# Performance work log

Measured on AMD Instinct MI355X. Metric: run time of the kernel, lower is better.

Reference implementation:

```python
import jax, jax.numpy as jnp
import numpy as np

H = 1536      # hidden_size
V = 128       # input_size == output_size (char vocab)
ML = 128      # MAX_LENGTH
SOS = 0


def setup_inputs() -> dict:
    key = jax.random.key(0)
    ks = jax.random.split(key, 16)
    s = 1.0 / np.sqrt(H)
    f = lambda k, shp: jax.random.uniform(k, shp, jnp.float32, -s, s)
    return {
        "input_tensor": jax.random.randint(ks[0], (64,), 0, V),
        "max_length": ML,
        # encoder params
        "emb_enc": f(ks[1], (V, H)),
        "enc_Wih": f(ks[2], (3 * H, H)),
        "enc_Whh": f(ks[3], (3 * H, H)),
        "enc_bih": f(ks[4], (3 * H,)),
        "enc_bhh": f(ks[5], (3 * H,)),
        # decoder params
        "emb_dec": f(ks[6], (V, H)),
        "attn_W": f(ks[7], (ML + 1, 2 * H)),
        "attn_b": f(ks[8], (ML + 1,)),
        "comb_W": f(ks[9], (H, 2 * H)),
        "comb_b": f(ks[10], (H,)),
        "dec_Wih": f(ks[11], (3 * H, H)),
        "dec_Whh": f(ks[12], (3 * H, H)),
        "dec_bih": f(ks[13], (3 * H,)),
        "dec_bhh": f(ks[14], (3 * H,)),
        "out_W": f(ks[15], (V, H)),
        "out_b": jnp.zeros((V,), jnp.float32),
    }


def gru_step(x, h, Wih, Whh, bih, bhh):
    # PyTorch GRUCell math
    gi = Wih @ x + bih
    gh = Whh @ h + bhh
    i_r, i_z, i_n = jnp.split(gi, 3)
    h_r, h_z, h_n = jnp.split(gh, 3)
    r = jax.nn.sigmoid(i_r + h_r)
    z = jax.nn.sigmoid(i_z + h_z)
    n = jnp.tanh(i_n + r * h_n)
    return (1.0 - z) * n + z * h


def reference(input_tensor, max_length, emb_enc, enc_Wih, enc_Whh, enc_bih,
              enc_bhh, emb_dec, attn_W, attn_b, comb_W, comb_b, dec_Wih,
              dec_Whh, dec_bih, dec_bhh, out_W, out_b):
    L = input_tensor.shape[0]

    # ---- encoder: sequential GRU over input tokens ----
    def enc_step(h, tok):
        h = gru_step(emb_enc[tok], h, enc_Wih, enc_Whh, enc_bih, enc_bhh)
        return h, h
    h0 = jnp.zeros((H,), emb_enc.dtype)
    enc_h, enc_outs = jax.lax.scan(enc_step, h0, input_tensor)  # (L, H)
    encoder_outputs = jnp.zeros((max_length + 1, H), emb_enc.dtype).at[:L].set(enc_outs)

    # ---- attention decoder: greedy decode for max_length steps ----
    def dec_step(carry, _):
        h, tok = carry
        emb = emb_dec[tok]                                   # (H,)
        attn_logits = attn_W @ jnp.concatenate([emb, h]) + attn_b
        attn_w = jax.nn.softmax(attn_logits)                 # (ML+1,)
        context = attn_w @ encoder_outputs                   # (H,)
        x = jax.nn.relu(comb_W @ jnp.concatenate([emb, context]) + comb_b)
        h = gru_step(x, h, dec_Wih, dec_Whh, dec_bih, dec_bhh)
        logp = jax.nn.log_softmax(out_W @ h + out_b)         # (V,)
        nxt = jnp.argmax(logp).astype(tok.dtype)
        return (h, nxt), (logp, nxt)

    tok0 = jnp.asarray(SOS, input_tensor.dtype)
    _, (logps, tokens) = jax.lax.scan(dec_step, (enc_h, tok0), None,
                                      length=max_length)
    return logps, tokens  # (ML, V) log-probs, (ML,) greedy token ids
```

## Files before the change

kernel.cpp:

```cpp
#include <hip/hip_runtime.h>
#include <math.h>

#define H     1536
#define H3    4608
#define V     128
#define ML    128
#define MLP1  129
#define LEN   64
#define NBLK  256
#define NTHR  384
#define WPB   6
#define NWAVE (NBLK*WPB)
#define ACC_N    260
#define ACC_ROWS 8
#define ACC_STEP (ACC_ROWS*ACC_N)
#define TA_STRIDE 132

#define SCALEF     1099511627776.0f
#define INV_SCALED 9.094947017729282379150390625e-13

#define OFF_BAR 0
#define OFF_ZB  4096
#define OFF_ACC 10240
#define OFF_HS  2156800
#define OFF_XS  2943232
#define OFF_XE  3729664
#define OFF_GI  4122880
#define OFF_EO  5302528
#define OFF_M   5695744
#define OFF_TA  6088960
#define OFF_TC  6156544
#define OFF_CT  6942976
#define WS_END  8540416
#define MEMSET_BYTES 2156800

__device__ __forceinline__ float uc_ldf(const float* p){
  return __hip_atomic_load(p, __ATOMIC_RELAXED, __HIP_MEMORY_SCOPE_AGENT);
}
__device__ __forceinline__ void uc_stf(float* p, float v){
  __hip_atomic_store(p, v, __ATOMIC_RELAXED, __HIP_MEMORY_SCOPE_AGENT);
}
__device__ __forceinline__ unsigned uc_ldu(const unsigned* p){
  return __hip_atomic_load(p, __ATOMIC_RELAXED, __HIP_MEMORY_SCOPE_AGENT);
}
__device__ __forceinline__ void uc_stu64(unsigned long long* p, unsigned long long v){
  __hip_atomic_store(p, v, __ATOMIC_RELAXED, __HIP_MEMORY_SCOPE_AGENT);
}

__device__ __forceinline__ float wred(float v){
  #pragma unroll
  for(int s=32;s>0;s>>=1) v += __shfl_xor(v, s, 64);
  return v;
}

__device__ __forceinline__ void load6(const float* p, int lane, float4 r[6]){
  const float4* q = (const float4*)p;
  #pragma unroll
  for(int c=0;c<6;c++) r[c] = q[c*64+lane];
}
__device__ __forceinline__ float dot4(const float4 a, const float4 b){
  return a.x*b.x + a.y*b.y + a.z*b.z + a.w*b.w;
}
__device__ __forceinline__ float dot6(const float4 a[6], const float4 b[6]){
  float s=0.f;
  #pragma unroll
  for(int c=0;c<6;c++) s += dot4(a[c], b[c]);
  return s;
}

__device__ __forceinline__ void gbar(unsigned* bar, int rnd){
  __syncthreads();
  if(threadIdx.x==0){
    unsigned* grp  = bar + 32*(1 + (blockIdx.x >> 4));
    unsigned* root = bar;
    unsigned a = __hip_atomic_fetch_add(grp, 1u, __ATOMIC_RELAXED, __HIP_MEMORY_SCOPE_AGENT);
    if((a & 0xFFFFu) == (unsigned)(16*rnd + 15)){
      unsigned ra = __hip_atomic_fetch_add(root, 1u, __ATOMIC_RELAXED, __HIP_MEMORY_SCOPE_AGENT);
      if(ra != (unsigned)(16*rnd + 15)){
        while(uc_ldu(root) < (unsigned)(16*(rnd+1)))
          __builtin_amdgcn_s_sleep(1);
      }
      __hip_atomic_fetch_add(grp, 0x10000u, __ATOMIC_RELAXED, __HIP_MEMORY_SCOPE_AGENT);
    } else {
      while((uc_ldu(grp) >> 16) < (unsigned)(rnd+1))
        __builtin_amdgcn_s_sleep(1);
    }
  }
  __syncthreads();
}

__global__ __launch_bounds__(NTHR, 2)
void seq2seq_kernel(const int* __restrict__ toks,
                    const float* __restrict__ emb_enc,
                    const float* __restrict__ enc_Wih,
                    const float* __restrict__ enc_Whh,
                    const float* __restrict__ enc_bih,
                    const float* __restrict__ enc_bhh,
                    const float* __restrict__ emb_dec,
                    const float* __restrict__ attn_W,
                    const float* __restrict__ attn_b,
                    const float* __restrict__ comb_W,
                    const float* __restrict__ comb_b,
                    const float* __restrict__ dec_Wih,
                    const float* __restrict__ dec_Whh,
                    const float* __restrict__ dec_bih,
                    const float* __restrict__ dec_bhh,
                    const float* __restrict__ out_W,
                    const float* __restrict__ out_b,
                    float* __restrict__ out,
                    char* __restrict__ ws)
{
  const int tid = threadIdx.x, b = blockIdx.x;
  const int lane = tid & 63, w = tid >> 6;
  const int gw = b*WPB + w;
  int rnd = 0;

  unsigned* bar = (unsigned*)ws;
  float* zb = (float*)(ws + OFF_ZB);
  unsigned long long* accseq = (unsigned long long*)(ws + OFF_ACC);
  float* hseq = (float*)(ws + OFF_HS);
  float* xseq = (float*)(ws + OFF_XS);
  float* Xe = (float*)(ws + OFF_XE);
  float* Gi = (float*)(ws + OFF_GI);
  float* EO = (float*)(ws + OFF_EO);
  float* Mm = (float*)(ws + OFF_M);
  float* tA = (float*)(ws + OFF_TA);
  float* tC = (float*)(ws + OFF_TC);
  float* cT = (float*)(ws + OFF_CT);

  __shared__ float smem[WPB*3*H];
  __shared__ float sh[H];
  __shared__ float sx[H];
  __shared__ float scT[WPB*ACC_N];
  __shared__ float sv[ACC_N];
  __shared__ float shc[8];

  for(int idx = b*NTHR + tid; idx < LEN*H; idx += NBLK*NTHR){
    int t = idx / H, k = idx - t*H;
    uc_stf(&Xe[idx], emb_enc[toks[t]*H + k]);
  }
  for(int idx = b*NTHR + tid; idx < H*257; idx += NBLK*NTHR){
    int i = idx / 257, c = idx - i*257;
    float v = (c < MLP1) ? attn_W[(size_t)c*2*H + H + i]
                         : out_W[(size_t)(c-MLP1)*H + i];
    uc_stf(&cT[(size_t)i*ACC_N + c], v);
  }
  gbar(bar, rnd++);

  {
    int r = b*18 + w*3;
    for(int g=0; g<4; g++){
      __syncthreads();
      for(int idx = tid; idx < 16*384; idx += NTHR)
        ((float4*)smem)[idx] = ((const float4*)Xe)[g*16*384 + idx];
      __syncthreads();
      float4 rv0[6], rv1[6], rv2[6];
      load6(enc_Wih + (size_t)r*H,     lane, rv0);
      load6(enc_Wih + (size_t)(r+1)*H, lane, rv1);
      load6(enc_Wih + (size_t)(r+2)*H, lane, rv2);
      float a0[16], a1[16], a2[16];
      #pragma unroll
      for(int t2=0;t2<16;t2++){ a0[t2]=0.f; a1[t2]=0.f; a2[t2]=0.f; }
      #pragma unroll
      for(int c=0;c<6;c++){
        #pragma unroll
        for(int t2=0;t2<16;t2++){
          float4 x = ((float4*)smem)[t2*384 + c*64 + lane];
          a0[t2] += dot4(rv0[c], x);
          a1[t2] += dot4(rv1[c], x);
          a2[t2] += dot4(rv2[c], x);
        }
      }
      float bi0 = enc_bih[r], bi1 = enc_bih[r+1], bi2 = enc_bih[r+2];
      #pragma unroll
      for(int t2=0;t2<16;t2++){
        float s0 = wred(a0[t2]), s1 = wred(a1[t2]), s2 = wred(a2[t2]);
        if(lane==0){
          uc_stf(&Gi[(size_t)(g*16+t2)*H3 + r    ], s0 + bi0);
          uc_stf(&Gi[(size_t)(g*16+t2)*H3 + r + 1], s1 + bi1);
          uc_stf(&Gi[(size_t)(g*16+t2)*H3 + r + 2], s2 + bi2);
        }
      }
    }
  }
  gbar(bar, rnd++);

  {
    int i = gw;
    float4 rv[6]; load6(comb_W + (size_t)i*2*H, lane, rv);
    for(int g=0; g<8; g++){
      __syncthreads();
      for(int idx = tid; idx < 16*384; idx += NTHR)
        ((float4*)smem)[idx] = ((const float4*)emb_dec)[g*16*384 + idx];
      __syncthreads();
      float a0[16];
      #pragma unroll
      for(int t2=0;t2<16;t2++) a0[t2]=0.f;
      #pragma unroll
      for(int c=0;c<6;c++){
        #pragma unroll
        for(int t2=0;t2<16;t2++){
          float4 x = ((float4*)smem)[t2*384 + c*64 + lane];
          a0[t2] += dot4(rv[c], x);
        }
      }
      #pragma unroll
      for(int t2=0;t2<16;t2++){
        float s = wred(a0[t2]);
        if(lane==0) uc_stf(&tC[(size_t)(g*16+t2)*H + i], s);
      }
    }
  }

  for(int task = gw; task < MLP1*V; task += NWAVE){
    int j = task >> 7, v = task & 127;
    float4 av[6]; load6(attn_W + (size_t)j*2*H, lane, av);
    float4 ev[6]; load6(emb_dec + (size_t)v*H, lane, ev);
    float s = wred(dot6(av, ev));
    if(lane==0) uc_stf(&tA[v*TA_STRIDE + j], s);
  }
  gbar(bar, rnd++);

  for(int idx = tid; idx < 18*384; idx += NTHR){
    int row = idx/384, k4 = idx - row*384;
    int w2 = row/3, gate = row - w2*3;
    ((float4*)smem)[idx] =
      ((const float4*)enc_Whh)[((size_t)gate*H + b*WPB + w2)*384 + k4];
  }
  const int i0 = gw;
  float gi0 = Gi[(size_t)lane*H3 + i0];
  float gi1 = Gi[(size_t)lane*H3 + i0 + H];
  float gi2 = Gi[(size_t)lane*H3 + i0 + 2*H];
  float eb0 = enc_bhh[i0], eb1 = enc_bhh[i0+H], eb2 = enc_bhh[i0+2*H];
  __syncthreads();

  for(int t=0; t<LEN; t++){
    const float* hprev = (t==0) ? zb : (EO + (size_t)(t-1)*H);
    ((float4*)sh)[tid] = ((const float4*)hprev)[tid];
    __syncthreads();
    float4 hv[6]; load6(sh, lane, hv);
    float s[3];
    #pragma unroll
    for(int g=0; g<3; g++){
      const float4* sr = (const float4*)smem + (w*3+g)*384;
      float t0=0.f;
      #pragma unroll
      for(int c=0;c<6;c++) t0 += dot4(sr[c*64+lane], hv[c]);
      s[g] = wred(t0);
    }
    float ir = __shfl(gi0, t, 64), iz = __shfl(gi1, t, 64), in_ = __shfl(gi2, t, 64);
    if(lane==0){
      float r = 1.f/(1.f+expf(-(ir + s[0] + eb0)));
      float z = 1.f/(1.f+expf(-(iz + s[1] + eb1)));
      float n = tanhf(in_ + r*(s[2] + eb2));
      float hn = (1.f-z)*n + z*sh[i0];
      uc_stf(&EO[(size_t)t*H + i0], hn);
    }
    gbar(bar, rnd++);
  }

  {
    int i = gw;
    float4 rv[6]; load6(comb_W + (size_t)i*2*H + H, lane, rv);
    for(int g=0; g<4; g++){
      __syncthreads();
      for(int idx = tid; idx < 16*384; idx += NTHR)
        ((float4*)smem)[idx] = ((const float4*)EO)[g*16*384 + idx];
      __syncthreads();
      float a0[16];
      #pragma unroll
      for(int t2=0;t2<16;t2++) a0[t2]=0.f;
      #pragma unroll
      for(int c=0;c<6;c++){
        #pragma unroll
        for(int t2=0;t2<16;t2++){
          float4 x = ((float4*)smem)[t2*384 + c*64 + lane];
          a0[t2] += dot4(rv[c], x);
        }
      }
      #pragma unroll
      for(int t2=0;t2<16;t2++){
        float s = wred(a0[t2]);
        if(lane==0) uc_stf(&Mm[(size_t)i*64 + g*16 + t2], s);
      }
    }
  }

  if(gw < MLP1){
    int j = gw;
    float4 av[6]; load6(attn_W + (size_t)j*2*H + H, lane, av);
    float4 hv[6]; load6(EO + (size_t)(LEN-1)*H, lane, hv);
    float s = wred(dot6(av, hv));
    if(lane==0)
      uc_stu64(&accseq[j], (unsigned long long)(long long)rintf(s*SCALEF));
  }
  for(int idx = tid; idx < 18*384; idx += NTHR){
    int row = idx/384, k4 = idx - row*384;
    int w2 = row/3, gate = row - w2*3;
    ((float4*)smem)[idx] =
      ((const float4*)dec_Whh)[((size_t)gate*H + b*WPB + w2)*384 + k4];
  }
  for(int idx = tid; idx < WPB*ACC_N; idx += NTHR){
    int w2 = idx / ACC_N, c = idx - w2*ACC_N;
    scT[idx] = cT[(size_t)(b*WPB + w2)*ACC_N + c];
  }
  gbar(bar, rnd++);

  const int i = gw;
  float4 wx0[6], wx1[6], wx2[6];
  load6(dec_Wih + (size_t)i*H,         lane, wx0);
  load6(dec_Wih + ((size_t)H + i)*H,   lane, wx1);
  load6(dec_Wih + ((size_t)2*H + i)*H, lane, wx2);
  const float mreg = Mm[(size_t)i*64 + lane];
  const float ct0 = tC[(size_t)lane*H + i];
  const float ct1 = tC[(size_t)(64+lane)*H + i];
  const float ib0 = dec_bih[i], ib1 = dec_bih[i+H], ib2 = dec_bih[i+2*H];
  const float hb0 = dec_bhh[i], hb1 = dec_bhh[i+H], hb2 = dec_bhh[i+2*H];
  const float cb  = comb_b[i];
  const float ob0 = out_b[lane], ob1 = out_b[64+lane];
  const float ab0 = attn_b[lane], ab1 = attn_b[64+lane], ab2 = attn_b[128];

  for(int t=0; t<ML; t++){
    const float* hprev = (t==0) ? (EO + (size_t)(LEN-1)*H) : (hseq + (size_t)(t-1)*H);
    const unsigned long long* accC = accseq + (size_t)t*ACC_STEP;
    unsigned long long* accA = accseq + (size_t)(t+1)*ACC_STEP;

    ((float4*)sh)[tid] = ((const float4*)hprev)[tid];
    if(tid < 257){
      long long s = 0;
      #pragma unroll
      for(int r2=0; r2<ACC_ROWS; r2++)
        s += ((const long long*)accC)[r2*ACC_N + tid];
      sv[tid] = (float)((double)s * INV_SCALED);
    }
    __syncthreads();

    float4 hv[6]; load6(sh, lane, hv);
    float sWh[3];
    #pragma unroll
    for(int g=0; g<3; g++){
      const float4* sp = (const float4*)smem + (w*3+g)*384;
      float t1=0.f;
      #pragma unroll
      for(int c=0;c<6;c++) t1 += dot4(sp[c*64+lane], hv[c]);
      sWh[g] = wred(t1);
    }

    float o0 = sv[MLP1+lane]    + ob0;
    float o1 = sv[MLP1+64+lane] + ob1;
    float mv; int mi;
    if(o0 >= o1){ mv=o0; mi=lane; } else { mv=o1; mi=64+lane; }
    #pragma unroll
    for(int sft=32; sft>0; sft>>=1){
      float ov = __shfl_xor(mv, sft, 64);
      int   oi = __shfl_xor(mi, sft, 64);
      if(ov > mv || (ov == mv && oi < mi)){ mv = ov; mi = oi; }
    }
    const int tok = (t==0) ? 0 : mi;
    if(b==0 && w==0 && t>0){
      float e0w = expf(o0-mv) + expf(o1-mv);
      float ss = wred(e0w);
      float lse = mv + logf(ss);
      out[(size_t)(t-1)*V + lane]      = o0 - lse;
      out[(size_t)(t-1)*V + 64 + lane] = o1 - lse;
      if(lane==0) out[(size_t)ML*V + (t-1)] = (float)tok;
    }

    float v0 = sv[lane]      + tA[tok*TA_STRIDE + lane]      + ab0;
    float v1 = sv[64+lane]   + tA[tok*TA_STRIDE + 64 + lane] + ab1;
    float v2 = (lane==0) ? (sv[128] + tA[tok*TA_STRIDE + 128] + ab2) : -1e30f;
    float m0 = fmaxf(fmaxf(v0, v1), v2);
    #pragma unroll
    for(int sft=32; sft>0; sft>>=1) m0 = fmaxf(m0, __shfl_xor(m0, sft, 64));
    float e0 = expf(v0 - m0);
    float esum = e0 + expf(v1 - m0) + ((lane==0) ? expf(v2 - m0) : 0.f);
    esum = wred(esum);
    const float invd = 1.f/esum;

    {
      float s = wred(mreg * e0);
      float ctv = (tok < 64) ? __shfl(ct0, tok, 64) : __shfl(ct1, tok-64, 64);
      if(lane==0)
        uc_stf(&xseq[(size_t)t*H + i], fmaxf(ctv + s*invd + cb, 0.f));
    }
    gbar(bar, rnd++);

    ((float4*)sx)[tid] = ((const float4*)(xseq + (size_t)t*H))[tid];
    __syncthreads();
    float4 xv[6]; load6(sx, lane, xv);
    float t0=0.f, t1=0.f, t2=0.f;
    #pragma unroll
    for(int c=0;c<6;c++){
      t0 += dot4(wx0[c], xv[c]);
      t1 += dot4(wx1[c], xv[c]);
      t2 += dot4(wx2[c], xv[c]);
    }
    float sWx0 = wred(t0), sWx1 = wred(t1), sWx2 = wred(t2);
    if(lane==0){
      float r = 1.f/(1.f+expf(-(sWx0+ib0 + sWh[0]+hb0)));
      float z = 1.f/(1.f+expf(-(sWx1+ib1 + sWh[1]+hb1)));
      float n = tanhf(sWx2+ib2 + r*(sWh[2]+hb2));
      float hn = (1.f-z)*n + z*sh[i];
      uc_stf(&hseq[(size_t)t*H + i], hn);
      shc[w] = hn;
    }
    __syncthreads();
    if(tid < 257){
      float s = 0.f;
      #pragma unroll
      for(int w2=0; w2<WPB; w2++)
        s += scT[w2*ACC_N + tid] * shc[w2];
      atomicAdd(&accA[(b & (ACC_ROWS-1))*ACC_N + tid],
                (unsigned long long)(long long)rintf(s*SCALEF));
    }
    gbar(bar, rnd++);
  }

  if(b==0){
    const unsigned long long* accC = accseq + (size_t)ML*ACC_STEP;
    if(tid < 257){
      long long s = 0;
      #pragma unroll
      for(int r2=0; r2<ACC_ROWS; r2++)
        s += ((const long long*)accC)[r2*ACC_N + tid];
      sv[tid] = (float)((double)s * INV_SCALED);
    }
    __syncthreads();
    if(w==0){
      float o0 = sv[MLP1+lane]    + ob0;
      float o1 = sv[MLP1+64+lane] + ob1;
      float mv; int mi;
      if(o0 >= o1){ mv=o0; mi=lane; } else { mv=o1; mi=64+lane; }
      #pragma unroll
      for(int sft=32; sft>0; sft>>=1){
        float ov = __shfl_xor(mv, sft, 64);
        int   oi = __shfl_xor(mi, sft, 64);
        if(ov > mv || (ov == mv && oi < mi)){ mv = ov; mi = oi; }
      }
      float e0 = expf(o0-mv) + expf(o1-mv);
      float ss = wred(e0);
      float lse = mv + logf(ss);
      out[(size_t)(ML-1)*V + lane]      = o0 - lse;
      out[(size_t)(ML-1)*V + 64 + lane] = o1 - lse;
      if(lane==0) out[(size_t)ML*V + (ML-1)] = (float)mi;
    }
  }
}

extern "C" void kernel_launch(void* const* d_in, const int* in_sizes, int n_in,
                              void* d_out, int out_size, void* d_ws, size_t ws_size,
                              hipStream_t stream){
  (void)in_sizes; (void)n_in; (void)out_size; (void)ws_size;
  const int*   toks    = (const int*)  d_in[0];
  const float* emb_enc = (const float*)d_in[2];
  const float* enc_Wih = (const float*)d_in[3];
  const float* enc_Whh = (const float*)d_in[4];
  const float* enc_bih = (const float*)d_in[5];
  const float* enc_bhh = (const float*)d_in[6];
  const float* emb_dec = (const float*)d_in[7];
  const float* attn_W  = (const float*)d_in[8];
  const float* attn_b  = (const float*)d_in[9];
  const float* comb_W  = (const float*)d_in[10];
  const float* comb_b  = (const float*)d_in[11];
  const float* dec_Wih = (const float*)d_in[12];
  const float* dec_Whh = (const float*)d_in[13];
  const float* dec_bih = (const float*)d_in[14];
  const float* dec_bhh = (const float*)d_in[15];
  const float* out_W   = (const float*)d_in[16];
  const float* out_b   = (const float*)d_in[17];
  float* outp = (float*)d_out;
  char*  ws   = (char*)d_ws;

  hipMemsetAsync(d_ws, 0, MEMSET_BYTES, stream);

  void* args[] = { &toks, &emb_enc, &enc_Wih, &enc_Whh, &enc_bih, &enc_bhh,
                   &emb_dec, &attn_W, &attn_b, &comb_W, &comb_b,
                   &dec_Wih, &dec_Whh, &dec_bih, &dec_bhh, &out_W, &out_b,
                   &outp, &ws };
  hipLaunchCooperativeKernel((void*)seq2seq_kernel, dim3(NBLK), dim3(NTHR),
                             args, 0, stream);
}
```

Baseline: 2.274 ms.

## Compute combined input redundantly per block to drop a grid barrier per decode step

Each block now computes the full combined/attention input vector x itself, reading a transposed M matrix (64xH) and the token row of tC with float4 loads, instead of each wave computing one element and exchanging through global memory. This removes one grid-wide barrier and the xseq round trip per decode step. In exchange every block reads about 400KB of M per step, so L2 traffic rises sharply. Launch bounds also drop to one block per SM to give more registers.

```diff
diff --git a/kernel.cpp b/kernel.cpp
--- a/kernel.cpp
+++ b/kernel.cpp
@@ -89,7 +89,7 @@
   __syncthreads();
 }
 
-__global__ __launch_bounds__(NTHR, 2)
+__global__ __launch_bounds__(NTHR, 1)
 void seq2seq_kernel(const int* __restrict__ toks,
                     const float* __restrict__ emb_enc,
                     const float* __restrict__ enc_Wih,
@@ -119,11 +119,10 @@
   float* zb = (float*)(ws + OFF_ZB);
   unsigned long long* accseq = (unsigned long long*)(ws + OFF_ACC);
   float* hseq = (float*)(ws + OFF_HS);
-  float* xseq = (float*)(ws + OFF_XS);
   float* Xe = (float*)(ws + OFF_XE);
   float* Gi = (float*)(ws + OFF_GI);
   float* EO = (float*)(ws + OFF_EO);
-  float* Mm = (float*)(ws + OFF_M);
+  float* Mt = (float*)(ws + OFF_M);
   float* tA = (float*)(ws + OFF_TA);
   float* tC = (float*)(ws + OFF_TC);
   float* cT = (float*)(ws + OFF_CT);
@@ -133,6 +132,7 @@
   __shared__ float sx[H];
   __shared__ float scT[WPB*ACC_N];
   __shared__ float sv[ACC_N];
+  __shared__ float se[64];
   __shared__ float shc[8];
 
   for(int idx = b*NTHR + tid; idx < LEN*H; idx += NBLK*NTHR){
@@ -281,7 +281,7 @@
       #pragma unroll
       for(int t2=0;t2<16;t2++){
         float s = wred(a0[t2]);
-        if(lane==0) uc_stf(&Mm[(size_t)i*64 + g*16 + t2], s);
+        if(lane==0) uc_stf(&Mt[(size_t)(g*16+t2)*H + i], s);
       }
     }
   }
@@ -311,14 +311,14 @@
   load6(dec_Wih + (size_t)i*H,         lane, wx0);
   load6(dec_Wih + ((size_t)H + i)*H,   lane, wx1);
   load6(dec_Wih + ((size_t)2*H + i)*H, lane, wx2);
-  const float mreg = Mm[(size_t)i*64 + lane];
-  const float ct0 = tC[(size_t)lane*H + i];
-  const float ct1 = tC[(size_t)(64+lane)*H + i];
   const float ib0 = dec_bih[i], ib1 = dec_bih[i+H], ib2 = dec_bih[i+2*H];
   const float hb0 = dec_bhh[i], hb1 = dec_bhh[i+H], hb2 = dec_bhh[i+2*H];
-  const float cb  = comb_b[i];
+  const float4 cb4 = ((const float4*)comb_b)[tid];
   const float ob0 = out_b[lane], ob1 = out_b[64+lane];
   const float ab0 = attn_b[lane], ab1 = attn_b[64+lane], ab2 = attn_b[128];
+
+  const float4* Mt4 = (const float4*)Mt;
+  const float4* tC4 = (const float4*)tC;
 
   for(int t=0; t<ML; t++){
     const float* hprev = (t==0) ? (EO + (size_t)(LEN-1)*H) : (hseq + (size_t)(t-1)*H);
@@ -357,14 +357,6 @@
       if(ov > mv || (ov == mv && oi < mi)){ mv = ov; mi = oi; }
     }
     const int tok = (t==0) ? 0 : mi;
-    if(b==0 && w==0 && t>0){
-      float e0w = expf(o0-mv) + expf(o1-mv);
-      float ss = wred(e0w);
-      float lse = mv + logf(ss);
-      out[(size_t)(t-1)*V + lane]      = o0 - lse;
-      out[(size_t)(t-1)*V + 64 + lane] = o1 - lse;
-      if(lane==0) out[(size_t)ML*V + (t-1)] = (float)tok;
-    }
 
     float v0 = sv[lane]      + tA[tok*TA_STRIDE + lane]      + ab0;
     float v1 = sv[64+lane]   + tA[tok*TA_STRIDE + 64 + lane] + ab1;
@@ -376,17 +368,37 @@
     float esum = e0 + expf(v1 - m0) + ((lane==0) ? expf(v2 - m0) : 0.f);
     esum = wred(esum);
     const float invd = 1.f/esum;
+    if(w==0) se[lane] = e0 * invd;
+
+    if(b==0 && w==0 && t>0){
+      float e0w = expf(o0-mv) + expf(o1-mv);
+      float ss = wred(e0w);
+      float lse = mv + logf(ss);
+      out[(size_t)(t-1)*V + lane]      = o0 - lse;
+      out[(size_t)(t-1)*V + 64 + lane] = o1 - lse;
+      if(lane==0) out[(size_t)ML*V + (t-1)] = (float)tok;
+    }
+    __syncthreads();
 
     {
-      float s = wred(mreg * e0);
-      float ctv = (tok < 64) ? __shfl(ct0, tok, 64) : __shfl(ct1, tok-64, 64);
-      if(lane==0)
-        uc_stf(&xseq[(size_t)t*H + i], fmaxf(ctv + s*invd + cb, 0.f));
-    }
-    gbar(bar, rnd++);
-
-    ((float4*)sx)[tid] = ((const float4*)(xseq + (size_t)t*H))[tid];
-    __syncthreads();
+      float cx=0.f, cy=0.f, cz=0.f, cw=0.f;
+      #pragma unroll 8
+      for(int j=0;j<64;j++){
+        float4 m = Mt4[(size_t)j*384 + tid];
+        float g = se[j];
+        cx = fmaf(m.x, g, cx); cy = fmaf(m.y, g, cy);
+        cz = fmaf(m.z, g, cz); cw = fmaf(m.w, g, cw);
+      }
+      float4 tc = tC4[(size_t)tok*384 + tid];
+      float4 xr;
+      xr.x = fmaxf(tc.x + cx + cb4.x, 0.f);
+      xr.y = fmaxf(tc.y + cy + cb4.y, 0.f);
+      xr.z = fmaxf(tc.z + cz + cb4.z, 0.f);
+      xr.w = fmaxf(tc.w + cw + cb4.w, 0.f);
+      ((float4*)sx)[tid] = xr;
+    }
+    __syncthreads();
+
     float4 xv[6]; load6(sx, lane, xv);
     float t0=0.f, t1=0.f, t2=0.f;
     #pragma unroll
```

Measured after the change: 2.420 ms. +6.4%, slower.
